# Performance work log

Measured on AMD Instinct MI355X. Metric: run time of the kernel, lower is better.

Reference implementation:

```python
import jax, jax.numpy as jnp
import numpy as np
import math

B, S, D = 2, 2048, 2048
H, KV, HD = 32, 8, 64
G = H // KV  # 4
BASE = 10000.0


def _rope_tables(seq_len, dtype):
    inv_freq = 1.0 / (BASE ** (jnp.arange(0, HD, 2, dtype=jnp.float32) / HD))
    t = jnp.arange(seq_len, dtype=jnp.float32)
    freqs = jnp.outer(t, inv_freq)               # [S, HD/2]
    emb = jnp.concatenate([freqs, freqs], -1)     # [S, HD]
    return jnp.cos(emb).astype(dtype), jnp.sin(emb).astype(dtype)


def _rotate_half(x):
    x1, x2 = x[..., : HD // 2], x[..., HD // 2 :]
    return jnp.concatenate([-x2, x1], axis=-1)


def setup_inputs() -> dict:
    key = jax.random.key(0)
    ks = jax.random.split(key, 5)
    s = 0.02
    return {
        "hidden_states": jax.random.normal(ks[0], (B, S, D), jnp.float32),
        "Wq": jax.random.normal(ks[1], (D, H * HD), jnp.float32) * s,
        "Wk": jax.random.normal(ks[2], (D, KV * HD), jnp.float32) * s,
        "Wv": jax.random.normal(ks[3], (D, KV * HD), jnp.float32) * s,
        "Wo": jax.random.normal(ks[4], (D, D), jnp.float32) * s,
    }


def reference(hidden_states, Wq, Wk, Wv, Wo):
    b, s, _ = hidden_states.shape
    q = (hidden_states @ Wq).reshape(b, s, H, HD).transpose(0, 2, 1, 3)   # [B,H,S,HD]
    k = (hidden_states @ Wk).reshape(b, s, KV, HD).transpose(0, 2, 1, 3)  # [B,KV,S,HD]
    v = (hidden_states @ Wv).reshape(b, s, KV, HD).transpose(0, 2, 1, 3)

    cos, sin = _rope_tables(s, hidden_states.dtype)  # [S, HD]
    cos = cos[None, None]
    sin = sin[None, None]
    q = q * cos + _rotate_half(q) * sin
    k = k * cos + _rotate_half(k) * sin

    # GQA: repeat kv heads to match query heads
    k = jnp.repeat(k, G, axis=1)  # [B,H,S,HD]
    v = jnp.repeat(v, G, axis=1)

    scores = jnp.einsum("bhqd,bhkd->bhqk", q, k) / math.sqrt(HD)
    causal = jnp.triu(jnp.full((s, s), float("-inf"), dtype=scores.dtype), k=1)
    scores = scores + causal
    attn = jax.nn.softmax(scores, axis=-1)
    out = jnp.einsum("bhqk,bhkd->bhqd", attn, v)          # [B,H,S,HD]
    out = out.transpose(0, 2, 1, 3).reshape(b, s, H * HD)  # [B,S,D]
    return out @ Wo
```

## Files before the change

kernel.cpp:

```cpp
#include <hip/hip_runtime.h>
#include <hip/hip_bf16.h>

#define BATCH  2
#define SEQ    2048
#define DMODEL 2048
#define NHEADS 32
#define NKV    8
#define HDIM   64
#define ROWS   (BATCH * SEQ)
#define NQKV   3072

typedef __attribute__((ext_vector_type(8))) short bf16x8;
typedef __attribute__((ext_vector_type(4))) float floatx4;

__device__ __forceinline__ float b2f(unsigned short u) {
    union { unsigned int i; float f; } x; x.i = ((unsigned int)u) << 16; return x.f;
}
__device__ __forceinline__ unsigned short f2b(float f) {
    union { float f; unsigned int i; } x; x.f = f;
    unsigned int r = x.i + 0x7fffu + ((x.i >> 16) & 1u);
    return (unsigned short)(r >> 16);
}
__device__ __forceinline__ unsigned int pkbf(float a, float b) {
    union { __hip_bfloat162 h; unsigned int u; } x;
    x.h = __float22bfloat162_rn(make_float2(a, b));
    return x.u;
}

#define GLD16(g, l) __builtin_amdgcn_global_load_lds( \
    (const __attribute__((address_space(1))) unsigned int*)(g), \
    (__attribute__((address_space(3))) unsigned int*)(l), 16, 0, 0)

__global__ void rope_table(float2* __restrict__ tab) {
    int idx = blockIdx.x * 256 + threadIdx.x;
    int i = idx & 31, t = idx >> 5;
    float inv = powf(10000.0f, -(float)i * (1.0f / 32.0f));
    float s, c;
    sincosf((float)t * inv, &s, &c);
    tab[idx] = make_float2(c, s);
}

template <bool BF16_OUT, bool DO_ROPE>
__global__ __launch_bounds__(256) void mfma_gemm(const unsigned short* __restrict__ A,
                                                 const unsigned short* __restrict__ Bt,
                                                 void* __restrict__ Cout,
                                                 const float2* __restrict__ rtab,
                                                 int M, int N, int K) {
    __shared__ unsigned short As[3][128 * 32];
    __shared__ unsigned short Bs[3][128 * 32];

    const int tid  = threadIdx.x;
    const int wave = tid >> 6;
    const int lane = tid & 63;
    const int m0 = blockIdx.y * 128;
    const int n0 = blockIdx.x * 128;
    const int wr0 = (wave >> 1) * 64;
    const int wc0 = (wave & 1) * 64;

    const int srow = wave * 32 + (lane >> 2);
    const int skc  = (lane & 3) * 8;
    const unsigned short* Ap0 = A  + (size_t)(m0 + srow) * K + skc;
    const unsigned short* Ap1 = Ap0 + (size_t)16 * K;
    const unsigned short* Bp0 = Bt + (size_t)(n0 + srow) * K + skc;
    const unsigned short* Bp1 = Bp0 + (size_t)16 * K;

    const int fr = lane & 15;
    const int fk = (lane >> 4) * 8;

    floatx4 acc[4][4];
    #pragma unroll
    for (int r = 0; r < 4; ++r)
        #pragma unroll
        for (int c = 0; c < 4; ++c)
            #pragma unroll
            for (int g = 0; g < 4; ++g) acc[r][c][g] = 0.f;

    const int NT = K >> 5;

    auto stage = [&](int t, int buf) {
        unsigned short* Ab = &As[buf][wave * 1024];
        unsigned short* Bb = &Bs[buf][wave * 1024];
        const int k0 = t * 32;
        GLD16(Ap0 + k0, Ab);
        GLD16(Ap1 + k0, Ab + 512);
        GLD16(Bp0 + k0, Bb);
        GLD16(Bp1 + k0, Bb + 512);
    };

    stage(0, 0);
    stage(1, 1);
    asm volatile("s_waitcnt vmcnt(4)" ::: "memory");
    __builtin_amdgcn_s_barrier();
    __builtin_amdgcn_sched_barrier(0);

    int cur = 0, nx2 = 2;
    for (int T = 0; T < NT; ++T) {
        if (T + 2 < NT) stage(T + 2, nx2);

        const unsigned short* Asb = &As[cur][0];
        const unsigned short* Bsb = &Bs[cur][0];
        bf16x8 af[4], bfr[4];
        #pragma unroll
        for (int r = 0; r < 4; ++r)
            af[r] = *(const bf16x8*)&Asb[(wr0 + r * 16 + fr) * 32 + fk];
        #pragma unroll
        for (int c = 0; c < 4; ++c)
            bfr[c] = *(const bf16x8*)&Bsb[(wc0 + c * 16 + fr) * 32 + fk];
        #pragma unroll
        for (int r = 0; r < 4; ++r)
            #pragma unroll
            for (int c = 0; c < 4; ++c)
                acc[r][c] = __builtin_amdgcn_mfma_f32_16x16x32_bf16(af[r], bfr[c], acc[r][c], 0, 0, 0);

        if (T + 1 < NT) {
            if (T + 2 < NT)
                asm volatile("s_waitcnt vmcnt(4)" ::: "memory");
            else
                asm volatile("s_waitcnt vmcnt(0)" ::: "memory");
            __builtin_amdgcn_s_barrier();
            __builtin_amdgcn_sched_barrier(0);
        }
        cur = (cur == 2) ? 0 : cur + 1;
        nx2 = (nx2 == 2) ? 0 : nx2 + 1;
    }

    const int erow = (lane >> 4) * 4;
    const int ecol = lane & 15;

    if (DO_ROPE) {
        const int colb = n0 + wc0;
        if (colb < 2560) {
            const float scale = (colb < 2048) ? 0.125f : 1.0f;
            #pragma unroll
            for (int r = 0; r < 4; ++r)
                #pragma unroll
                for (int g = 0; g < 4; ++g) {
                    int t = (m0 + wr0 + r * 16 + erow + g) & (SEQ - 1);
                    float2 cs0 = rtab[t * 32 + ecol];
                    float2 cs1 = rtab[t * 32 + ecol + 16];
                    float a0 = acc[r][0][g], a2 = acc[r][2][g];
                    acc[r][0][g] = (a0 * cs0.x - a2 * cs0.y) * scale;
                    acc[r][2][g] = (a2 * cs0.x + a0 * cs0.y) * scale;
                    float a1 = acc[r][1][g], a3 = acc[r][3][g];
                    acc[r][1][g] = (a1 * cs1.x - a3 * cs1.y) * scale;
                    acc[r][3][g] = (a3 * cs1.x + a1 * cs1.y) * scale;
                }
        }
    }

    #pragma unroll
    for (int r = 0; r < 4; ++r)
        #pragma unroll
        for (int c = 0; c < 4; ++c)
            #pragma unroll
            for (int g = 0; g < 4; ++g) {
                int row = m0 + wr0 + r * 16 + erow + g;
                int col = n0 + wc0 + c * 16 + ecol;
                if (BF16_OUT)
                    ((unsigned short*)Cout)[(size_t)row * N + col] = f2b(acc[r][c][g]);
                else
                    ((float*)Cout)[(size_t)row * N + col] = acc[r][c][g];
            }
}

__global__ __launch_bounds__(256) void transpose_cast_all(const float* __restrict__ Wq,
                                                          const float* __restrict__ Wk,
                                                          const float* __restrict__ Wv,
                                                          const float* __restrict__ Wo,
                                                          unsigned short* __restrict__ Wt,
                                                          unsigned short* __restrict__ Wot) {
    __shared__ float t[32][33];
    int bx = blockIdx.x;
    const float* src; unsigned short* dst; int N, nb;
    if (bx < 64)      { src = Wq; dst = Wt;                          N = 2048; nb = bx; }
    else if (bx < 80) { src = Wk; dst = Wt + (size_t)2048 * DMODEL;  N = 512;  nb = bx - 64; }
    else if (bx < 96) { src = Wv; dst = Wt + (size_t)2560 * DMODEL;  N = 512;  nb = bx - 80; }
    else              { src = Wo; dst = Wot;                         N = 2048; nb = bx - 96; }
    const int n0 = nb * 32, k0 = blockIdx.y * 32;
    const int tx = threadIdx.x & 31, ty = threadIdx.x >> 5;
    #pragma unroll
    for (int i = 0; i < 32; i += 8)
        t[ty + i][tx] = src[(size_t)(k0 + ty + i) * N + n0 + tx];
    __syncthreads();
    #pragma unroll
    for (int i = 0; i < 32; i += 8)
        dst[(size_t)(n0 + ty + i) * DMODEL + k0 + tx] = f2b(t[tx][ty + i]);
}

__global__ void cast_f32_to_bf16(const float* __restrict__ src,
                                 unsigned short* __restrict__ dst, int n) {
    int i = (blockIdx.x * 256 + threadIdx.x) * 8;
    if (i >= n) return;
    float4 a = *(const float4*)(src + i);
    float4 b = *(const float4*)(src + i + 4);
    uint4 o;
    o.x = pkbf(a.x, a.y); o.y = pkbf(a.z, a.w);
    o.z = pkbf(b.x, b.y); o.w = pkbf(b.z, b.w);
    *(uint4*)(dst + i) = o;
}

__global__ __launch_bounds__(256, 3) void attn_mfma(const unsigned short* __restrict__ QKV,
                                                    unsigned short* __restrict__ Ctx) {
    __shared__ unsigned short Ks[2][64][72];
    __shared__ unsigned short Vts[2][64][72];
    __shared__ unsigned short Ps[4][16][72];

    const int tid  = threadIdx.x;
    const int wave = tid >> 6;
    const int lane = tid & 63;
    const int px = blockIdx.x;
    const int h  = blockIdx.y;
    const int b  = blockIdx.z;
    const int kvh = h >> 2;

    const int fr = lane & 15;
    const int fg = lane >> 4;
    const size_t base = (size_t)(b * SEQ) * NQKV;

    const int krow = tid >> 2, kc0 = (tid & 3) * 16;
    const int vp2 = tid & 31, vh0 = (tid >> 5) * 8;
    const unsigned short* kbase = QKV + base + (size_t)krow * NQKV + 2048 + kvh * HDIM + kc0;
    const unsigned short* vbase = QKV + base + (size_t)(2 * vp2) * NQKV + 2560 + kvh * HDIM + vh0;

    #pragma unroll 1
    for (int t = 0; t < 2; ++t) {
        const int qb = (t == 0) ? (31 - px) : px;
        const int wbase = qb * 64 + wave * 16;

        bf16x8 qf[2];
        #pragma unroll
        for (int ks = 0; ks < 2; ++ks)
            qf[ks] = *(const bf16x8*)(QKV + base + (size_t)(wbase + fr) * NQKV
                                      + h * HDIM + ks * 32 + fg * 8);

        float l = 0.f;
        floatx4 acc[4];
        #pragma unroll
        for (int j2 = 0; j2 < 4; ++j2)
            #pragma unroll
            for (int g = 0; g < 4; ++g) acc[j2][g] = 0.f;

        const int nkb = qb + 1;

        bf16x8 kr0 = *(const bf16x8*)kbase;
        bf16x8 kr1 = *(const bf16x8*)(kbase + 8);
        bf16x8 v0  = *(const bf16x8*)vbase;
        bf16x8 v1  = *(const bf16x8*)(vbase + NQKV);

        for (int kb = 0; kb < nkb; ++kb) {
            const int pb = kb & 1;
            *(bf16x8*)&Ks[pb][krow][kc0]     = kr0;
            *(bf16x8*)&Ks[pb][krow][kc0 + 8] = kr1;
            #pragma unroll
            for (int j = 0; j < 8; ++j) {
                unsigned int w = (unsigned int)(unsigned short)v0[j]
                               | ((unsigned int)(unsigned short)v1[j] << 16);
                *(unsigned int*)&Vts[pb][vh0 + j][2 * vp2] = w;
            }
            {
                int nx = (kb + 1 < nkb) ? kb + 1 : kb;
                const unsigned short* kp = kbase + (size_t)(nx * 64) * NQKV;
                const unsigned short* vp = vbase + (size_t)(nx * 64) * NQKV;
                kr0 = *(const bf16x8*)kp;
                kr1 = *(const bf16x8*)(kp + 8);
                v0  = *(const bf16x8*)vp;
                v1  = *(const bf16x8*)(vp + NQKV);
            }
            __syncthreads();

            const bool skip = (kb * 64 > wbase + 15);
            if (!skip) {
                const bool needMask = (kb * 64 + 63 > wbase);

                floatx4 sc[4];
                #pragma unroll
                for (int j = 0; j < 4; ++j)
                    #pragma unroll
                    for (int g = 0; g < 4; ++g) sc[j][g] = 0.f;
                __builtin_amdgcn_s_setprio(1);
                #pragma unroll
                for (int ks = 0; ks < 2; ++ks) {
                    #pragma unroll
                    for (int j = 0; j < 4; ++j) {
                        bf16x8 kf = *(const bf16x8*)&Ks[pb][j * 16 + fr][ks * 32 + fg * 8];
                        sc[j] = __builtin_amdgcn_mfma_f32_16x16x32_bf16(kf, qf[ks], sc[j], 0, 0, 0);
                    }
                }
                __builtin_amdgcn_s_setprio(0);

                if (needMask) {
                    int qi = wbase + fr;
                    #pragma unroll
                    for (int j = 0; j < 4; ++j)
                        #pragma unroll
                        for (int g = 0; g < 4; ++g) {
                            int kj = kb * 64 + j * 16 + fg * 4 + g;
                            if (kj > qi) sc[j][g] = -1e30f;
                        }
                }

                #pragma unroll
                for (int j = 0; j < 4; ++j) {
                    #pragma unroll
                    for (int g = 0; g < 4; ++g) {
                        float e = __expf(sc[j][g]);
                        sc[j][g] = e;
                        l += e;
                    }
                    uint2 w;
                    w.x = pkbf(sc[j][0], sc[j][1]);
                    w.y = pkbf(sc[j][2], sc[j][3]);
                    *(uint2*)&Ps[wave][fr][j * 16 + fg * 4] = w;
                }

                __builtin_amdgcn_s_setprio(1);
                #pragma unroll
                for (int ks = 0; ks < 2; ++ks) {
                    bf16x8 pf = *(const bf16x8*)&Ps[wave][fr][ks * 32 + fg * 8];
                    #pragma unroll
                    for (int j2 = 0; j2 < 4; ++j2) {
                        bf16x8 vf = *(const bf16x8*)&Vts[pb][j2 * 16 + fr][ks * 32 + fg * 8];
                        acc[j2] = __builtin_amdgcn_mfma_f32_16x16x32_bf16(vf, pf, acc[j2], 0, 0, 0);
                    }
                }
                __builtin_amdgcn_s_setprio(0);
            }
        }
        __syncthreads();

        {
            float lt = l;
            lt += __shfl_xor(lt, 16);
            lt += __shfl_xor(lt, 32);
            float inv = 1.0f / lt;
            int q = wbase + fr;
            unsigned short* cp = Ctx + (size_t)(b * SEQ + q) * DMODEL + h * HDIM;
            #pragma unroll
            for (int j2 = 0; j2 < 4; ++j2) {
                uint2 w;
                w.x = pkbf(acc[j2][0] * inv, acc[j2][1] * inv);
                w.y = pkbf(acc[j2][2] * inv, acc[j2][3] * inv);
                *(uint2*)(cp + j2 * 16 + fg * 4) = w;
            }
        }
    }
}

extern "C" void kernel_launch(void* const* d_in, const int* in_sizes, int n_in,
                              void* d_out, int out_size, void* d_ws, size_t ws_size,
                              hipStream_t stream) {
    const float* X  = (const float*)d_in[0];
    const float* Wq = (const float*)d_in[1];
    const float* Wk = (const float*)d_in[2];
    const float* Wv = (const float*)d_in[3];
    const float* Wo = (const float*)d_in[4];
    float* out = (float*)d_out;

    unsigned short* Xb   = (unsigned short*)d_ws;
    unsigned short* Wt   = Xb + (size_t)ROWS * DMODEL;
    unsigned short* Wot  = Wt + (size_t)NQKV * DMODEL;
    unsigned short* QKVb = Wot + (size_t)DMODEL * DMODEL;
    unsigned short* Ctxb = QKVb + (size_t)ROWS * NQKV;
    float2* Rtab = (float2*)(Ctxb + (size_t)ROWS * DMODEL);

    rope_table<<<256, 256, 0, stream>>>(Rtab);
    cast_f32_to_bf16<<<(ROWS * DMODEL) / (8 * 256), 256, 0, stream>>>(X, Xb, ROWS * DMODEL);
    transpose_cast_all<<<dim3(160, 64), 256, 0, stream>>>(Wq, Wk, Wv, Wo, Wt, Wot);

    mfma_gemm<true, true><<<dim3(NQKV / 128, ROWS / 128), 256, 0, stream>>>(Xb, Wt, QKVb, Rtab, ROWS, NQKV, DMODEL);

    attn_mfma<<<dim3(SEQ / 128, NHEADS, BATCH), 256, 0, stream>>>(QKVb, Ctxb);

    mfma_gemm<false, false><<<dim3(DMODEL / 128, ROWS / 128), 256, 0, stream>>>(Ctxb, Wot, out, Rtab, ROWS, DMODEL, DMODEL);
}
```

Before: 336.6 us.

## Swizzle GEMM tiles, stage RoPE table in LDS, single-buffer attention K/V

The GEMM now remaps workgroup IDs in an XCD-style swizzle for better L2 locality. It also reuses its shared memory to stage the block's RoPE cos/sin rows before the epilogue, so the table is not read repeatedly from global memory. The attention kernel drops K/V double buffering in LDS and adds a barrier at the top of each iteration. This shrinks LDS so launch bounds can request 5 blocks per CU instead of 3, at the cost of an extra sync per key block.

```diff
diff --git a/kernel.cpp b/kernel.cpp
--- a/kernel.cpp
+++ b/kernel.cpp
@@ -46,14 +46,20 @@
                                                  void* __restrict__ Cout,
                                                  const float2* __restrict__ rtab,
                                                  int M, int N, int K) {
-    __shared__ unsigned short As[3][128 * 32];
-    __shared__ unsigned short Bs[3][128 * 32];
+    __shared__ __align__(16) unsigned char smem[49152];
+    unsigned short (*As)[4096] = (unsigned short (*)[4096])smem;
+    unsigned short (*Bs)[4096] = (unsigned short (*)[4096])(smem + 24576);
 
     const int tid  = threadIdx.x;
     const int wave = tid >> 6;
     const int lane = tid & 63;
-    const int m0 = blockIdx.y * 128;
-    const int n0 = blockIdx.x * 128;
+
+    const int nwg  = gridDim.x * gridDim.y;
+    const int wgid = blockIdx.y * gridDim.x + blockIdx.x;
+    const int swz  = (wgid & 7) * (nwg >> 3) + (wgid >> 3);
+    const int m0 = (swz / gridDim.x) * 128;
+    const int n0 = (swz % gridDim.x) * 128;
+
     const int wr0 = (wave >> 1) * 64;
     const int wc0 = (wave & 1) * 64;
 
@@ -128,6 +134,18 @@
     const int ecol = lane & 15;
 
     if (DO_ROPE) {
+        __syncthreads();
+        float2* tab = (float2*)smem;
+        {
+            int lr = tid >> 1, hf = (tid & 1) * 16;
+            int t  = (m0 + lr) & (SEQ - 1);
+            const float4* src = (const float4*)(rtab + (size_t)t * 32 + hf);
+            float4* dst = (float4*)(tab + lr * 32 + hf);
+            #pragma unroll
+            for (int u = 0; u < 8; ++u) dst[u] = src[u];
+        }
+        __syncthreads();
+
         const int colb = n0 + wc0;
         if (colb < 2560) {
             const float scale = (colb < 2048) ? 0.125f : 1.0f;
@@ -135,9 +153,9 @@
             for (int r = 0; r < 4; ++r)
                 #pragma unroll
                 for (int g = 0; g < 4; ++g) {
-                    int t = (m0 + wr0 + r * 16 + erow + g) & (SEQ - 1);
-                    float2 cs0 = rtab[t * 32 + ecol];
-                    float2 cs1 = rtab[t * 32 + ecol + 16];
+                    int lr = wr0 + r * 16 + erow + g;
+                    float2 cs0 = tab[lr * 32 + ecol];
+                    float2 cs1 = tab[lr * 32 + ecol + 16];
                     float a0 = acc[r][0][g], a2 = acc[r][2][g];
                     acc[r][0][g] = (a0 * cs0.x - a2 * cs0.y) * scale;
                     acc[r][2][g] = (a2 * cs0.x + a0 * cs0.y) * scale;
@@ -199,10 +217,10 @@
     *(uint4*)(dst + i) = o;
 }
 
-__global__ __launch_bounds__(256, 3) void attn_mfma(const unsigned short* __restrict__ QKV,
+__global__ __launch_bounds__(256, 5) void attn_mfma(const unsigned short* __restrict__ QKV,
                                                     unsigned short* __restrict__ Ctx) {
-    __shared__ unsigned short Ks[2][64][72];
-    __shared__ unsigned short Vts[2][64][72];
+    __shared__ unsigned short Ks[64][72];
+    __shared__ unsigned short Vts[64][72];
     __shared__ unsigned short Ps[4][16][72];
 
     const int tid  = threadIdx.x;
@@ -248,14 +266,14 @@
         bf16x8 v1  = *(const bf16x8*)(vbase + NQKV);
 
         for (int kb = 0; kb < nkb; ++kb) {
-            const int pb = kb & 1;
-            *(bf16x8*)&Ks[pb][krow][kc0]     = kr0;
-            *(bf16x8*)&Ks[pb][krow][kc0 + 8] = kr1;
+            __syncthreads();
+            *(bf16x8*)&Ks[krow][kc0]     = kr0;
+            *(bf16x8*)&Ks[krow][kc0 + 8] = kr1;
             #pragma unroll
             for (int j = 0; j < 8; ++j) {
                 unsigned int w = (unsigned int)(unsigned short)v0[j]
                                | ((unsigned int)(unsigned short)v1[j] << 16);
-                *(unsigned int*)&Vts[pb][vh0 + j][2 * vp2] = w;
+                *(unsigned int*)&Vts[vh0 + j][2 * vp2] = w;
             }
             {
                 int nx = (kb + 1 < nkb) ? kb + 1 : kb;
@@ -282,7 +300,7 @@
                 for (int ks = 0; ks < 2; ++ks) {
                     #pragma unroll
                     for (int j = 0; j < 4; ++j) {
-                        bf16x8 kf = *(const bf16x8*)&Ks[pb][j * 16 + fr][ks * 32 + fg * 8];
+                        bf16x8 kf = *(const bf16x8*)&Ks[j * 16 + fr][ks * 32 + fg * 8];
                         sc[j] = __builtin_amdgcn_mfma_f32_16x16x32_bf16(kf, qf[ks], sc[j], 0, 0, 0);
                     }
                 }
@@ -319,14 +337,13 @@
                     bf16x8 pf = *(const bf16x8*)&Ps[wave][fr][ks * 32 + fg * 8];
                     #pragma unroll
                     for (int j2 = 0; j2 < 4; ++j2) {
-                        bf16x8 vf = *(const bf16x8*)&Vts[pb][j2 * 16 + fr][ks * 32 + fg * 8];
+                        bf16x8 vf = *(const bf16x8*)&Vts[j2 * 16 + fr][ks * 32 + fg * 8];
                         acc[j2] = __builtin_amdgcn_mfma_f32_16x16x32_bf16(vf, pf, acc[j2], 0, 0, 0);
                     }
                 }
                 __builtin_amdgcn_s_setprio(0);
             }
         }
-        __syncthreads();
 
         {
             float lt = l;
```

New measurement: 304.7 us. 9.5% less time.
